# Optimization experiments

Measured on AMD Instinct MI355X. Metric: run time of the kernel, lower is better.

The kernel has to match this reference:

```python
import jax, jax.numpy as jnp
import numpy as np

N_NODES = 50000
N_EDGES = 800000
EMB = 128
HID = [128, 128]
OUT = 64
CE = 8  # stand-in for CROSS_ENTROPY_INDEXES: first 8 output columns get sigmoid


def _linear_params(key, d_in, d_out):
    k1, k2 = jax.random.split(key)
    s = 1.0 / np.sqrt(d_in)
    w = jax.random.uniform(k1, (d_in, d_out), minval=-s, maxval=s, dtype=jnp.float32)
    b = jax.random.uniform(k2, (d_out,), minval=-s, maxval=s, dtype=jnp.float32)
    return w, b


def setup_inputs() -> dict:
    key = jax.random.key(0)
    ks = jax.random.split(key, 16)
    z = jax.random.normal(ks[0], (N_NODES, EMB), dtype=jnp.float32)
    edge_index = jax.random.randint(ks[1], (2, N_EDGES), 0, N_NODES, dtype=jnp.int64)
    # SAGEConv params: neighbor weight (with bias) + root weight
    w1_n, b1 = _linear_params(ks[2], EMB, HID[0])
    w1_r, _ = _linear_params(ks[3], EMB, HID[0])
    w2_n, b2 = _linear_params(ks[4], HID[0], HID[1])
    w2_r, _ = _linear_params(ks[5], HID[0], HID[1])
    wf_n, bf = _linear_params(ks[6], HID[1], OUT)
    wf_r, _ = _linear_params(ks[7], HID[1], OUT)
    # initial residual linears: emb -> hid[1], emb -> out
    w_res1, b_res1 = _linear_params(ks[8], EMB, HID[1])
    w_res2, b_res2 = _linear_params(ks[9], EMB, OUT)
    return dict(z=z, edge_index=edge_index,
                w1_n=w1_n, w1_r=w1_r, b1=b1,
                w2_n=w2_n, w2_r=w2_r, b2=b2,
                wf_n=wf_n, wf_r=wf_r, bf=bf,
                w_res1=w_res1, b_res1=b_res1,
                w_res2=w_res2, b_res2=b_res2)


def _sage(x, src, dst, w_n, w_r, b, n_nodes):
    # mean-aggregate neighbor features at target nodes, then affine combine with root
    msg = x[src]                                        # [E, d]
    agg = jax.ops.segment_sum(msg, dst, num_segments=n_nodes)
    deg = jax.ops.segment_sum(jnp.ones_like(dst, dtype=x.dtype), dst, num_segments=n_nodes)
    mean = agg / jnp.maximum(deg, 1.0)[:, None]
    return mean @ w_n + x @ w_r + b


def reference(z, edge_index, w1_n, w1_r, b1, w2_n, w2_r, b2, wf_n, wf_r, bf,
              w_res1, b_res1, w_res2, b_res2):
    n = z.shape[0]
    src, dst = edge_index[0], edge_index[1]
    h = jax.nn.relu(_sage(z, src, dst, w1_n, w1_r, b1, n))
    # mid layer (dropout is identity in eval) + initial residual
    h = jax.nn.relu(_sage(h, src, dst, w2_n, w2_r, b2, n))
    h = h + (z @ w_res1 + b_res1)
    # final conv + final residual
    h = _sage(h, src, dst, wf_n, wf_r, bf, n)
    h = h + (z @ w_res2 + b_res2)
    # sigmoid on cross-entropy columns
    h = h.at[:, :CE].set(jax.nn.sigmoid(h[:, :CE]))
    return h
```

## Files before the change

### kernel.cpp

```cpp
#include <hip/hip_runtime.h>
#include <hip/hip_bf16.h>
#include <math.h>

#define NN 50000
#define NNP 50048
#define NE 800000
#define NB 391
#define EPB 6250

typedef short bf16x8 __attribute__((ext_vector_type(8)));
typedef float f32x4 __attribute__((ext_vector_type(4)));
typedef float f32x2 __attribute__((ext_vector_type(2)));
typedef unsigned short us4 __attribute__((ext_vector_type(4)));
typedef unsigned short us8 __attribute__((ext_vector_type(8)));
typedef unsigned int u32x4 __attribute__((ext_vector_type(4)));

__device__ __forceinline__ float bf2f(unsigned short u) {
  union { unsigned int i; float f; } x; x.i = ((unsigned int)u) << 16; return x.f;
}
__device__ __forceinline__ float u2f(unsigned int u) {
  union { unsigned int i; float f; } x; x.i = u; return x.f;
}
__device__ __forceinline__ unsigned short f2bf(float f) {
  union { float f; unsigned int i; } x; x.f = f;
  unsigned int i = x.i;
  unsigned int r = i + 0x7FFF + ((i >> 16) & 1);
  return (unsigned short)(r >> 16);
}
__device__ __forceinline__ unsigned long long pk64(f32x4 v) {
  union { us4 s; unsigned long long u; } x;
  x.s[0] = f2bf(v[0]); x.s[1] = f2bf(v[1]); x.s[2] = f2bf(v[2]); x.s[3] = f2bf(v[3]);
  return x.u;
}
__device__ __forceinline__ bf16x8 bfrag(const unsigned short* __restrict__ Bp, int idx, int lane) {
  return *(const bf16x8*)(Bp + (size_t)idx * 512 + lane * 8);
}

__device__ __forceinline__ int scan_incl_512(int v, int* s) {
  int t = threadIdx.x;
  s[t] = v; __syncthreads();
  for (int off = 1; off < 512; off <<= 1) {
    int x = (t >= off) ? s[t - off] : 0;
    __syncthreads();
    s[t] += x;
    __syncthreads();
  }
  return s[t];
}

__global__ __launch_bounds__(512) void bscat_kernel(const int* __restrict__ srcn,
                                                    const int* __restrict__ dstn,
                                                    const int* __restrict__ bhist,
                                                    int* __restrict__ gcur,
                                                    unsigned long long* __restrict__ ebuf) {
  __shared__ int sbuf[512];
  __shared__ int boff[NB];
  __shared__ int hist[NB];
  __shared__ int base[NB];
  int t = threadIdx.x;
  int v = (t < NB) ? bhist[t] : 0;
  int incl = scan_incl_512(v, sbuf);
  if (t < NB) { boff[t] = incl - v; hist[t] = 0; }
  __syncthreads();
  int e0 = blockIdx.x * EPB;
  for (int i = t; i < EPB; i += 512)
    atomicAdd(&hist[dstn[e0 + i] >> 7], 1);
  __syncthreads();
  for (int i = t; i < NB; i += 512) {
    int c = hist[i];
    base[i] = c ? (boff[i] + atomicAdd(&gcur[i], c)) : 0;
  }
  __syncthreads();
  for (int i = t; i < EPB; i += 512) {
    int s = srcn[e0 + i], d = dstn[e0 + i];
    int b = d >> 7;
    int pos = atomicSub(&hist[b], 1) - 1;
    ebuf[(size_t)base[b] + pos] = ((unsigned long long)(unsigned)d << 32) | (unsigned)s;
  }
}

__global__ __launch_bounds__(512) void bfill_kernel(const unsigned long long* __restrict__ ebuf,
                                                    const int* __restrict__ bhist,
                                                    int* __restrict__ rowoff,
                                                    int* __restrict__ csr) {
  __shared__ int sbuf[512];
  __shared__ int sb[2];
  __shared__ int ndeg[128], noff[128];
  int b = blockIdx.x;
  int t = threadIdx.x;
  int v = (t < NB) ? bhist[t] : 0;
  int incl = scan_incl_512(v, sbuf);
  if (t == b) { sb[0] = incl - v; sb[1] = v; }
  if (t < 128) ndeg[t] = 0;
  __syncthreads();
  int bo = sb[0], cnt = sb[1];
  for (int i = t; i < cnt; i += 512)
    atomicAdd(&ndeg[(int)(ebuf[bo + i] >> 32) & 127], 1);
  __syncthreads();
  if (t < 128) noff[t] = ndeg[t];
  __syncthreads();
  for (int off = 1; off < 128; off <<= 1) {
    int x = 0;
    if (t < 128 && t >= off) x = noff[t - off];
    __syncthreads();
    if (t < 128 && t >= off) noff[t] += x;
    __syncthreads();
  }
  if (t < 128) {
    int ex = noff[t] - ndeg[t];
    noff[t] = ex;
    int node = b * 128 + t;
    if (node < NN) rowoff[node] = bo + ex;
  }
  if (b == NB - 1 && t == 0) rowoff[NN] = NE;
  __syncthreads();
  for (int i = t; i < cnt; i += 512) {
    unsigned long long e = ebuf[bo + i];
    int dl = (int)(e >> 32) & 127;
    int pos = atomicSub(&ndeg[dl], 1) - 1;
    csr[bo + noff[dl] + pos] = (int)(unsigned)e;
  }
}

__global__ __launch_bounds__(256) void setup_kernel(
    const float* __restrict__ z, unsigned short* __restrict__ A1,
    const float* __restrict__ w1n, const float* __restrict__ w1r,
    const float* __restrict__ w2n, const float* __restrict__ w2r,
    const float* __restrict__ wfn, const float* __restrict__ wfr,
    const float* __restrict__ wr1, const float* __restrict__ wr2,
    unsigned short* __restrict__ Bp1, unsigned short* __restrict__ Bp2,
    unsigned short* __restrict__ Bp3,
    const int* __restrict__ dstn, int* __restrict__ bhist) {
  __shared__ int h[NB];
  int b = blockIdx.x;
  if (b < 6250) {
    int i = b * 256 + threadIdx.x;
    if (i >= NN * 128 / 4) return;
    int i4 = i * 4;
    int row = i4 >> 7, c = i4 & 127;
    f32x4 v = *(const f32x4*)(z + i4);
    us4 o = { f2bf(v[0]), f2bf(v[1]), f2bf(v[2]), f2bf(v[3]) };
    *(us4*)(A1 + (size_t)row * 256 + 128 + c) = o;
  } else if (b < 6314) {
    int g = (b - 6250) * 256 + threadIdx.x;
    unsigned short* D; int NT, fi;
    int which;
    if      (g < 10240) { fi = g;         D = Bp1; NT = 20; which = 1; }
    else if (g < 14336) { fi = g - 10240; D = Bp2; NT = 8;  which = 2; }
    else if (g < 16384) { fi = g - 14336; D = Bp3; NT = 4;  which = 3; }
    else return;
    int lane = fi & 63, t = fi >> 6;
    int nt = t % NT, k0i = t / NT;
    int m = lane & 15, q = lane >> 4;
    int kb = k0i * 32 + q * 8;
    int n = nt * 16 + m;
    int hi = (kb >= 128);
    int k0_ = kb - (hi ? 128 : 0);
    const float* W = nullptr; int Nseg = 128; int nn = n;
    if (which == 1) {
      if (n < 128)      { W = hi ? w1r : w1n; nn = n; Nseg = 128; }
      else if (n < 256) { W = hi ? wr1 : nullptr; nn = n - 128; Nseg = 128; }
      else              { W = hi ? wr2 : nullptr; nn = n - 256; Nseg = 64; }
    } else if (which == 2) { W = hi ? w2r : w2n; Nseg = 128; }
    else                   { W = hi ? wfr : wfn; Nseg = 64; }
    unsigned short o[8];
#pragma unroll
    for (int j = 0; j < 8; j++)
      o[j] = W ? f2bf(W[(size_t)(k0_ + j) * Nseg + nn]) : (unsigned short)0;
    *(us8*)(D + (size_t)fi * 8) = *(const us8*)o;
  } else {
    for (int i = threadIdx.x; i < NB; i += 256) h[i] = 0;
    __syncthreads();
    int e0 = (b - 6314) * EPB;
    for (int i = threadIdx.x; i < EPB; i += 256)
      atomicAdd(&h[dstn[e0 + i] >> 7], 1);
    __syncthreads();
    for (int i = threadIdx.x; i < NB; i += 256)
      if (h[i]) atomicAdd(&bhist[i], h[i]);
  }
}

__device__ __forceinline__ void agg_wave(const unsigned short* __restrict__ feat,
                                         unsigned short* __restrict__ outm,
                                         const int* __restrict__ rowoff,
                                         const int* __restrict__ csr, int node) {
  int lane = threadIdx.x & 63;
  int g = lane >> 4;
  int c = (lane & 15) << 3;
  int beg = rowoff[node], end = rowoff[node + 1];
  f32x2 a[4];
#pragma unroll
  for (int k = 0; k < 4; ++k) a[k] = (f32x2){0.f, 0.f};
  int e1 = end - 1;
  for (int j = beg + g; j < end; j += 16) {
    int j1 = (j + 4 < e1) ? j + 4 : e1;
    int j2 = (j + 8 < e1) ? j + 8 : e1;
    int j3 = (j + 12 < e1) ? j + 12 : e1;
    int s0 = csr[j], s1 = csr[j1], s2 = csr[j2], s3 = csr[j3];
    float w1 = (j + 4 < end) ? 1.f : 0.f;
    float w2 = (j + 8 < end) ? 1.f : 0.f;
    float w3 = (j + 12 < end) ? 1.f : 0.f;
    u32x4 v0 = *(const u32x4*)(feat + (size_t)s0 * 256 + c);
    u32x4 v1 = *(const u32x4*)(feat + (size_t)s1 * 256 + c);
    u32x4 v2 = *(const u32x4*)(feat + (size_t)s2 * 256 + c);
    u32x4 v3 = *(const u32x4*)(feat + (size_t)s3 * 256 + c);
#pragma unroll
    for (int k = 0; k < 4; ++k) {
      f32x2 x0 = (f32x2){u2f(v0[k] << 16), u2f(v0[k] & 0xffff0000u)};
      f32x2 x1 = (f32x2){u2f(v1[k] << 16), u2f(v1[k] & 0xffff0000u)};
      f32x2 x2 = (f32x2){u2f(v2[k] << 16), u2f(v2[k] & 0xffff0000u)};
      f32x2 x3 = (f32x2){u2f(v3[k] << 16), u2f(v3[k] & 0xffff0000u)};
      a[k] += x0;
      a[k] += x1 * w1;
      a[k] += x2 * w2;
      a[k] += x3 * w3;
    }
  }
#pragma unroll
  for (int k = 0; k < 4; ++k)
#pragma unroll
    for (int h2 = 0; h2 < 2; ++h2) {
      a[k][h2] += __shfl_xor(a[k][h2], 16, 64);
      a[k][h2] += __shfl_xor(a[k][h2], 32, 64);
    }
  if (g == 0) {
    float inv = 1.f / fmaxf((float)(end - beg), 1.f);
    unsigned int o[4];
#pragma unroll
    for (int k = 0; k < 4; ++k)
      o[k] = ((unsigned int)f2bf(a[k][1] * inv) << 16) | f2bf(a[k][0] * inv);
    *(u32x4*)(outm + (size_t)node * 256 + c) = *(const u32x4*)o;
  }
}

__global__ __launch_bounds__(512, 8) void agg_kernel(unsigned short* __restrict__ A,
                                                     const int* __restrict__ rowoff,
                                                     const int* __restrict__ csr) {
  int node = blockIdx.x * 8 + (threadIdx.x >> 6);
  agg_wave(A + 128, A, rowoff, csr, node);
}

__global__ __launch_bounds__(512, 8) void aggres1_kernel(
    unsigned short* __restrict__ A1,
    const unsigned short* __restrict__ Bp1,
    const float* __restrict__ br1, const float* __restrict__ br2,
    const int* __restrict__ rowoff, const int* __restrict__ csr,
    unsigned short* __restrict__ res1, unsigned short* __restrict__ res2) {
  int bx = blockIdx.x;
  if (bx < 6250) {
    int node = bx * 8 + (threadIdx.x >> 6);
    agg_wave(A1 + 128, A1, rowoff, csr, node);
    return;
  }
  int b = bx - 6250;
  int chunk = (b >= NB);
  int bb = b - chunk * NB;
  int tid = threadIdx.x;
  int w = tid >> 6, lane = tid & 63;
  int m = lane & 15, q = lane >> 4;
  int row = bb * 128 + w * 16 + m;
  const unsigned short* ar = A1 + (size_t)row * 256 + 128 + q * 8;
  bf16x8 af[4];
#pragma unroll
  for (int k = 0; k < 4; ++k) af[k] = *(const bf16x8*)(ar + k * 32);
  f32x4 acc[6];
#pragma unroll
  for (int t = 0; t < 6; ++t) acc[t] = (f32x4){0.f, 0.f, 0.f, 0.f};
#pragma unroll
  for (int k0i = 0; k0i < 4; ++k0i)
#pragma unroll
    for (int t = 0; t < 6; ++t)
      acc[t] = __builtin_amdgcn_mfma_f32_16x16x32_bf16(
          bfrag(Bp1, (k0i + 4) * 20 + 8 + chunk * 6 + t, lane), af[k0i], acc[t], 0, 0, 0);
  int src0 = m + ((q & 1) ? 32 : 0);
#pragma unroll
  for (int pl = 0; pl < 3; ++pl) {
    int P = chunk * 3 + pl;
    const float* bias; unsigned short* dst; int dstride, colb;
    if (P < 4) { bias = br1 + 32 * P;       dst = res1; dstride = 128; colb = 32 * P; }
    else       { bias = br2 + 32 * (P - 4); dst = res2; dstride = 64;  colb = 32 * (P - 4); }
    f32x4 v0 = acc[2 * pl], v1 = acc[2 * pl + 1];
    f32x4 bb0 = *(const f32x4*)(bias + 4 * q);
    f32x4 bb1 = *(const f32x4*)(bias + 16 + 4 * q);
#pragma unroll
    for (int r = 0; r < 4; ++r) { v0[r] += bb0[r]; v1[r] += bb1[r]; }
    unsigned long long d0 = pk64(v0), d1 = pk64(v1);
    unsigned long long a0 = __shfl(d0, src0, 64);
    unsigned long long b0 = __shfl(d0, src0 + 16, 64);
    unsigned long long a1 = __shfl(d1, src0, 64);
    unsigned long long b1v = __shfl(d1, src0 + 16, 64);
    unsigned long long lo = (q >> 1) ? a1 : a0;
    unsigned long long hi = (q >> 1) ? b1v : b0;
    if (row < NN) {
      unsigned long long ov[2] = { lo, hi };
      *(us8*)(dst + (size_t)row * dstride + colb + 8 * q) = *(const us8*)ov;
    }
  }
}

__global__ __launch_bounds__(256, 4) void gemm1h_kernel(
    const unsigned short* __restrict__ A1,
    const unsigned short* __restrict__ Bp1,
    const float* __restrict__ b1,
    unsigned short* __restrict__ A2) {
  int tid = threadIdx.x;
  int w = tid >> 6, lane = tid & 63;
  int m = lane & 15, q = lane >> 4;
  int row = blockIdx.x * 64 + w * 16 + m;
  const unsigned short* ar = A1 + (size_t)row * 256 + q * 8;
  bf16x8 af[8];
#pragma unroll
  for (int k = 0; k < 8; ++k) af[k] = *(const bf16x8*)(ar + k * 32);
  f32x4 acc[8];
#pragma unroll
  for (int t = 0; t < 8; ++t) acc[t] = (f32x4){0.f, 0.f, 0.f, 0.f};
#pragma unroll
  for (int k0i = 0; k0i < 8; ++k0i)
#pragma unroll
    for (int t = 0; t < 8; ++t)
      acc[t] = __builtin_amdgcn_mfma_f32_16x16x32_bf16(
          bfrag(Bp1, k0i * 20 + t, lane), af[k0i], acc[t], 0, 0, 0);
  int src0 = m + ((q & 1) ? 32 : 0);
#pragma unroll
  for (int p = 0; p < 4; ++p) {
    f32x4 v0 = acc[2 * p], v1 = acc[2 * p + 1];
    f32x4 bb0 = *(const f32x4*)(b1 + 32 * p + 4 * q);
    f32x4 bb1 = *(const f32x4*)(b1 + 32 * p + 16 + 4 * q);
#pragma unroll
    for (int r = 0; r < 4; ++r) {
      v0[r] = fmaxf(v0[r] + bb0[r], 0.f);
      v1[r] = fmaxf(v1[r] + bb1[r], 0.f);
    }
    unsigned long long d0 = pk64(v0), d1 = pk64(v1);
    unsigned long long a0 = __shfl(d0, src0, 64);
    unsigned long long b0 = __shfl(d0, src0 + 16, 64);
    unsigned long long a1 = __shfl(d1, src0, 64);
    unsigned long long b1v = __shfl(d1, src0 + 16, 64);
    unsigned long long lo = (q >> 1) ? a1 : a0;
    unsigned long long hi = (q >> 1) ? b1v : b0;
    if (row < NN) {
      unsigned long long ov[2] = { lo, hi };
      *(us8*)(A2 + (size_t)row * 256 + 128 + 32 * p + 8 * q) = *(const us8*)ov;
    }
  }
}

__global__ __launch_bounds__(256, 4) void gemm2_kernel(
    const unsigned short* __restrict__ A2,
    const unsigned short* __restrict__ Bp2,
    const float* __restrict__ b2,
    const unsigned short* __restrict__ res1,
    unsigned short* __restrict__ A3) {
  int tid = threadIdx.x;
  int w = tid >> 6, lane = tid & 63;
  int m = lane & 15, q = lane >> 4;
  int row = blockIdx.x * 64 + w * 16 + m;
  const unsigned short* ar = A2 + (size_t)row * 256 + q * 8;
  bf16x8 af[8];
#pragma unroll
  for (int k = 0; k < 8; ++k) af[k] = *(const bf16x8*)(ar + k * 32);
  f32x4 acc[8];
#pragma unroll
  for (int t = 0; t < 8; ++t) acc[t] = (f32x4){0.f, 0.f, 0.f, 0.f};
#pragma unroll
  for (int k0i = 0; k0i < 8; ++k0i)
#pragma unroll
    for (int t = 0; t < 8; ++t)
      acc[t] = __builtin_amdgcn_mfma_f32_16x16x32_bf16(
          bfrag(Bp2, k0i * 8 + t, lane), af[k0i], acc[t], 0, 0, 0);
  int src0 = m + ((q & 1) ? 32 : 0);
#pragma unroll
  for (int p = 0; p < 4; ++p) {
    f32x4 v0 = acc[2 * p], v1 = acc[2 * p + 1];
    f32x4 bb0 = *(const f32x4*)(b2 + 32 * p + 4 * q);
    f32x4 bb1 = *(const f32x4*)(b2 + 32 * p + 16 + 4 * q);
#pragma unroll
    for (int r = 0; r < 4; ++r) {
      v0[r] = fmaxf(v0[r] + bb0[r], 0.f);
      v1[r] = fmaxf(v1[r] + bb1[r], 0.f);
    }
    unsigned long long d0 = pk64(v0), d1 = pk64(v1);
    unsigned long long a0 = __shfl(d0, src0, 64);
    unsigned long long b0 = __shfl(d0, src0 + 16, 64);
    unsigned long long a1 = __shfl(d1, src0, 64);
    unsigned long long b1v = __shfl(d1, src0 + 16, 64);
    unsigned long long lo = (q >> 1) ? a1 : a0;
    unsigned long long hi = (q >> 1) ? b1v : b0;
    if (row < NN) {
      size_t off = 32 * p + 8 * q;
      us8 rv = *(const us8*)(res1 + (size_t)row * 128 + off);
      unsigned long long ov[2] = { lo, hi };
      unsigned short* e = (unsigned short*)ov;
#pragma unroll
      for (int r = 0; r < 8; ++r) e[r] = f2bf(bf2f(e[r]) + bf2f(rv[r]));
      *(us8*)(A3 + (size_t)row * 256 + 128 + off) = *(const us8*)ov;
    }
  }
}

__global__ __launch_bounds__(256, 4) void gemm3_kernel(
    const unsigned short* __restrict__ A3,
    const unsigned short* __restrict__ Bp3,
    const float* __restrict__ bias,
    const unsigned short* __restrict__ res2,
    float* __restrict__ out_f) {
  int tid = threadIdx.x;
  int w = tid >> 6, lane = tid & 63;
  int m = lane & 15, q = lane >> 4;
  int row = blockIdx.x * 64 + w * 16 + m;
  const unsigned short* ar = A3 + (size_t)row * 256 + q * 8;
  bf16x8 af[8];
#pragma unroll
  for (int k = 0; k < 8; ++k) af[k] = *(const bf16x8*)(ar + k * 32);
  f32x4 acc[4];
#pragma unroll
  for (int t = 0; t < 4; ++t) acc[t] = (f32x4){0.f, 0.f, 0.f, 0.f};
#pragma unroll
  for (int k0i = 0; k0i < 8; ++k0i)
#pragma unroll
    for (int t = 0; t < 4; ++t)
      acc[t] = __builtin_amdgcn_mfma_f32_16x16x32_bf16(
          bfrag(Bp3, k0i * 4 + t, lane), af[k0i], acc[t], 0, 0, 0);
  if (row >= NN) return;
  int cb = q * 4;
#pragma unroll
  for (int s = 0; s < 4; ++s) {
    int col = s * 16 + cb;
    f32x4 v = acc[s];
    f32x4 bb = *(const f32x4*)(bias + col);
    us4 rv = *(const us4*)(res2 + (size_t)row * 64 + col);
#pragma unroll
    for (int r = 0; r < 4; ++r) v[r] += bb[r] + bf2f(rv[r]);
    if (col < 8) {
#pragma unroll
      for (int r = 0; r < 4; ++r) v[r] = 1.f / (1.f + __expf(-v[r]));
    }
    *(f32x4*)(out_f + (size_t)row * 64 + col) = v;
  }
}

extern "C" void kernel_launch(void* const* d_in, const int* in_sizes, int n_in,
                              void* d_out, int out_size, void* d_ws, size_t ws_size,
                              hipStream_t stream) {
  const float* z   = (const float*)d_in[0];
  const int*   edge = (const int*)d_in[1];
  const int*   srcn = edge;
  const int*   dstn = edge + NE;
  const float* w1n = (const float*)d_in[2];
  const float* w1r = (const float*)d_in[3];
  const float* b1  = (const float*)d_in[4];
  const float* w2n = (const float*)d_in[5];
  const float* w2r = (const float*)d_in[6];
  const float* b2  = (const float*)d_in[7];
  const float* wfn = (const float*)d_in[8];
  const float* wfr = (const float*)d_in[9];
  const float* bfb = (const float*)d_in[10];
  const float* wr1 = (const float*)d_in[11];
  const float* br1 = (const float*)d_in[12];
  const float* wr2 = (const float*)d_in[13];
  const float* br2 = (const float*)d_in[14];
  float* out = (float*)d_out;

  char* p = (char*)d_ws;
  auto alloc = [&](size_t bytes) { char* r = p; p += (bytes + 255) & ~255ull; return r; };
  int* rowoff = (int*)alloc((size_t)(NN + 1) * 4);
  int* bhist  = (int*)alloc((size_t)2 * NB * 4);
  int* gcur   = bhist + NB;
  int* csr    = (int*)alloc((size_t)NE * 4);
  unsigned short* A1 = (unsigned short*)alloc((size_t)NNP * 256 * 2);
  unsigned short* A2 = (unsigned short*)alloc((size_t)NNP * 256 * 2);
  unsigned short* res1 = (unsigned short*)alloc((size_t)NN * 128 * 2);
  unsigned short* res2 = (unsigned short*)alloc((size_t)NN * 64 * 2);
  unsigned short* Bp1 = (unsigned short*)alloc(10240 * 8 * 2);
  unsigned short* Bp2 = (unsigned short*)alloc(4096 * 8 * 2);
  unsigned short* Bp3 = (unsigned short*)alloc(2048 * 8 * 2);
  unsigned short* A3 = A1;
  unsigned long long* ebuf = (unsigned long long*)res1;

  hipMemsetAsync(bhist, 0, (size_t)2 * NB * 4, stream);
  setup_kernel<<<6442, 256, 0, stream>>>(z, A1, w1n, w1r, w2n, w2r, wfn, wfr, wr1, wr2,
                                         Bp1, Bp2, Bp3, dstn, bhist);
  bscat_kernel<<<128, 512, 0, stream>>>(srcn, dstn, bhist, gcur, ebuf);
  bfill_kernel<<<NB, 512, 0, stream>>>(ebuf, bhist, rowoff, csr);

  const int ggemm = NNP / 64;

  aggres1_kernel<<<6250 + 2 * NB, 512, 0, stream>>>(A1, Bp1, br1, br2, rowoff, csr, res1, res2);
  gemm1h_kernel<<<ggemm, 256, 0, stream>>>(A1, Bp1, b1, A2);

  agg_kernel<<<6250, 512, 0, stream>>>(A2, rowoff, csr);
  gemm2_kernel<<<ggemm, 256, 0, stream>>>(A2, Bp2, b2, res1, A3);

  agg_kernel<<<6250, 512, 0, stream>>>(A3, rowoff, csr);
  gemm3_kernel<<<ggemm, 256, 0, stream>>>(A3, Bp3, bfb, res2, out);
}
```

Before: 279.3 us.

## Project before aggregating in final layer and process two nodes per wave

The final SAGE layer now multiplies the hidden features by the neighbor weight inside gemm2 (mean is linear, so mean(x)W = mean(xW)), which lets the third aggregation gather 64-wide instead of 128-wide rows. A new agg64 kernel handles that narrower gather, and gemm3 then only multiplies the root half and adds the aggregated projection. The 128-wide aggregation is restructured so each wave handles two nodes at once, with clamped indices, to raise memory-level parallelism, and launch bounds drop to 4 waves per EU. Row guards on stores are removed by padding the residual buffers to NNP. The extra projection adds MFMA work to gemm2, and rounding the projected features to bf16 before the mean slightly changes numerics.

Measured after the change: 279.4 us. Within noise of the previous version (+0.1%).

```diff
diff --git a/kernel.cpp b/kernel.cpp
--- a/kernel.cpp
+++ b/kernel.cpp
@@ -180,46 +180,131 @@
   }
 }
 
-__device__ __forceinline__ void agg_wave(const unsigned short* __restrict__ feat,
-                                         unsigned short* __restrict__ outm,
-                                         const int* __restrict__ rowoff,
-                                         const int* __restrict__ csr, int node) {
+__device__ __forceinline__ void agg_wave2(const unsigned short* __restrict__ feat,
+                                          unsigned short* __restrict__ outm,
+                                          const int* __restrict__ rowoff,
+                                          const int* __restrict__ csr, int n0) {
   int lane = threadIdx.x & 63;
   int g = lane >> 4;
   int c = (lane & 15) << 3;
+  int begA = rowoff[n0], begB = rowoff[n0 + 1], endB = rowoff[n0 + 2];
+  int endA = begB;
+  f32x2 aA[4], aB[4];
+#pragma unroll
+  for (int k = 0; k < 4; ++k) { aA[k] = (f32x2){0.f, 0.f}; aB[k] = (f32x2){0.f, 0.f}; }
+  int e1A = endA - 1 > begA ? endA - 1 : begA;
+  int e1B = endB - 1 > begB ? endB - 1 : begB;
+  if (e1A >= NE) e1A = NE - 1;
+  if (e1B >= NE) e1B = NE - 1;
+  int jA = begA + g, jB = begB + g;
+  while (jA < endA || jB < endB) {
+    int iA0 = jA      < e1A ? jA      : e1A;
+    int iA1 = jA + 4  < e1A ? jA + 4  : e1A;
+    int iA2 = jA + 8  < e1A ? jA + 8  : e1A;
+    int iA3 = jA + 12 < e1A ? jA + 12 : e1A;
+    int iB0 = jB      < e1B ? jB      : e1B;
+    int iB1 = jB + 4  < e1B ? jB + 4  : e1B;
+    int iB2 = jB + 8  < e1B ? jB + 8  : e1B;
+    int iB3 = jB + 12 < e1B ? jB + 12 : e1B;
+    int sA0 = csr[iA0], sA1 = csr[iA1], sA2 = csr[iA2], sA3 = csr[iA3];
+    int sB0 = csr[iB0], sB1 = csr[iB1], sB2 = csr[iB2], sB3 = csr[iB3];
+    float wA0 = (jA      < endA) ? 1.f : 0.f;
+    float wA1 = (jA + 4  < endA) ? 1.f : 0.f;
+    float wA2 = (jA + 8  < endA) ? 1.f : 0.f;
+    float wA3 = (jA + 12 < endA) ? 1.f : 0.f;
+    float wB0 = (jB      < endB) ? 1.f : 0.f;
+    float wB1 = (jB + 4  < endB) ? 1.f : 0.f;
+    float wB2 = (jB + 8  < endB) ? 1.f : 0.f;
+    float wB3 = (jB + 12 < endB) ? 1.f : 0.f;
+    u32x4 vA0 = *(const u32x4*)(feat + (size_t)sA0 * 256 + c);
+    u32x4 vA1 = *(const u32x4*)(feat + (size_t)sA1 * 256 + c);
+    u32x4 vA2 = *(const u32x4*)(feat + (size_t)sA2 * 256 + c);
+    u32x4 vA3 = *(const u32x4*)(feat + (size_t)sA3 * 256 + c);
+    u32x4 vB0 = *(const u32x4*)(feat + (size_t)sB0 * 256 + c);
+    u32x4 vB1 = *(const u32x4*)(feat + (size_t)sB1 * 256 + c);
+    u32x4 vB2 = *(const u32x4*)(feat + (size_t)sB2 * 256 + c);
+    u32x4 vB3 = *(const u32x4*)(feat + (size_t)sB3 * 256 + c);
+#pragma unroll
+    for (int k = 0; k < 4; ++k) {
+      aA[k] += (f32x2){u2f(vA0[k] << 16), u2f(vA0[k] & 0xffff0000u)} * wA0;
+      aA[k] += (f32x2){u2f(vA1[k] << 16), u2f(vA1[k] & 0xffff0000u)} * wA1;
+      aA[k] += (f32x2){u2f(vA2[k] << 16), u2f(vA2[k] & 0xffff0000u)} * wA2;
+      aA[k] += (f32x2){u2f(vA3[k] << 16), u2f(vA3[k] & 0xffff0000u)} * wA3;
+      aB[k] += (f32x2){u2f(vB0[k] << 16), u2f(vB0[k] & 0xffff0000u)} * wB0;
+      aB[k] += (f32x2){u2f(vB1[k] << 16), u2f(vB1[k] & 0xffff0000u)} * wB1;
+      aB[k] += (f32x2){u2f(vB2[k] << 16), u2f(vB2[k] & 0xffff0000u)} * wB2;
+      aB[k] += (f32x2){u2f(vB3[k] << 16), u2f(vB3[k] & 0xffff0000u)} * wB3;
+    }
+    jA += 16; jB += 16;
+  }
+#pragma unroll
+  for (int k = 0; k < 4; ++k)
+#pragma unroll
+    for (int h2 = 0; h2 < 2; ++h2) {
+      aA[k][h2] += __shfl_xor(aA[k][h2], 16, 64);
+      aA[k][h2] += __shfl_xor(aA[k][h2], 32, 64);
+      aB[k][h2] += __shfl_xor(aB[k][h2], 16, 64);
+      aB[k][h2] += __shfl_xor(aB[k][h2], 32, 64);
+    }
+  if (g == 0) {
+    float invA = 1.f / fmaxf((float)(endA - begA), 1.f);
+    float invB = 1.f / fmaxf((float)(endB - begB), 1.f);
+    unsigned int oA[4], oB[4];
+#pragma unroll
+    for (int k = 0; k < 4; ++k) {
+      oA[k] = ((unsigned int)f2bf(aA[k][1] * invA) << 16) | f2bf(aA[k][0] * invA);
+      oB[k] = ((unsigned int)f2bf(aB[k][1] * invB) << 16) | f2bf(aB[k][0] * invB);
+    }
+    *(u32x4*)(outm + (size_t)n0 * 256 + c) = *(const u32x4*)oA;
+    *(u32x4*)(outm + (size_t)(n0 + 1) * 256 + c) = *(const u32x4*)oB;
+  }
+}
+
+__global__ __launch_bounds__(512, 4) void agg_kernel(unsigned short* __restrict__ A,
+                                                     const int* __restrict__ rowoff,
+                                                     const int* __restrict__ csr) {
+  int n0 = (blockIdx.x * 8 + (threadIdx.x >> 6)) * 2;
+  agg_wave2(A + 128, A, rowoff, csr, n0);
+}
+
+__device__ __forceinline__ void agg64_wave(const unsigned short* __restrict__ feat,
+                                           unsigned short* __restrict__ outm,
+                                           const int* __restrict__ rowoff,
+                                           const int* __restrict__ csr, int node) {
+  int lane = threadIdx.x & 63;
+  int g = lane >> 3;
+  int c = (lane & 7) << 3;
   int beg = rowoff[node], end = rowoff[node + 1];
   f32x2 a[4];
 #pragma unroll
   for (int k = 0; k < 4; ++k) a[k] = (f32x2){0.f, 0.f};
-  int e1 = end - 1;
-  for (int j = beg + g; j < end; j += 16) {
-    int j1 = (j + 4 < e1) ? j + 4 : e1;
-    int j2 = (j + 8 < e1) ? j + 8 : e1;
-    int j3 = (j + 12 < e1) ? j + 12 : e1;
+  int e1 = end - 1 > beg ? end - 1 : beg;
+  if (e1 >= NE) e1 = NE - 1;
+  for (int j = beg + g; j < end; j += 32) {
+    int j1 = (j + 8  < e1) ? j + 8  : e1;
+    int j2 = (j + 16 < e1) ? j + 16 : e1;
+    int j3 = (j + 24 < e1) ? j + 24 : e1;
     int s0 = csr[j], s1 = csr[j1], s2 = csr[j2], s3 = csr[j3];
-    float w1 = (j + 4 < end) ? 1.f : 0.f;
-    float w2 = (j + 8 < end) ? 1.f : 0.f;
-    float w3 = (j + 12 < end) ? 1.f : 0.f;
+    float w1 = (j + 8  < end) ? 1.f : 0.f;
+    float w2 = (j + 16 < end) ? 1.f : 0.f;
+    float w3 = (j + 24 < end) ? 1.f : 0.f;
     u32x4 v0 = *(const u32x4*)(feat + (size_t)s0 * 256 + c);
     u32x4 v1 = *(const u32x4*)(feat + (size_t)s1 * 256 + c);
     u32x4 v2 = *(const u32x4*)(feat + (size_t)s2 * 256 + c);
     u32x4 v3 = *(const u32x4*)(feat + (size_t)s3 * 256 + c);
 #pragma unroll
     for (int k = 0; k < 4; ++k) {
-      f32x2 x0 = (f32x2){u2f(v0[k] << 16), u2f(v0[k] & 0xffff0000u)};
-      f32x2 x1 = (f32x2){u2f(v1[k] << 16), u2f(v1[k] & 0xffff0000u)};
-      f32x2 x2 = (f32x2){u2f(v2[k] << 16), u2f(v2[k] & 0xffff0000u)};
-      f32x2 x3 = (f32x2){u2f(v3[k] << 16), u2f(v3[k] & 0xffff0000u)};
-      a[k] += x0;
-      a[k] += x1 * w1;
-      a[k] += x2 * w2;
-      a[k] += x3 * w3;
+      a[k] += (f32x2){u2f(v0[k] << 16), u2f(v0[k] & 0xffff0000u)};
+      a[k] += (f32x2){u2f(v1[k] << 16), u2f(v1[k] & 0xffff0000u)} * w1;
+      a[k] += (f32x2){u2f(v2[k] << 16), u2f(v2[k] & 0xffff0000u)} * w2;
+      a[k] += (f32x2){u2f(v3[k] << 16), u2f(v3[k] & 0xffff0000u)} * w3;
     }
   }
 #pragma unroll
   for (int k = 0; k < 4; ++k)
 #pragma unroll
     for (int h2 = 0; h2 < 2; ++h2) {
+      a[k][h2] += __shfl_xor(a[k][h2], 8, 64);
       a[k][h2] += __shfl_xor(a[k][h2], 16, 64);
       a[k][h2] += __shfl_xor(a[k][h2], 32, 64);
     }
@@ -233,26 +318,26 @@
   }
 }
 
-__global__ __launch_bounds__(512, 8) void agg_kernel(unsigned short* __restrict__ A,
-                                                     const int* __restrict__ rowoff,
-                                                     const int* __restrict__ csr) {
+__global__ __launch_bounds__(512, 8) void agg64_kernel(unsigned short* __restrict__ A1,
+                                                       const int* __restrict__ rowoff,
+                                                       const int* __restrict__ csr) {
   int node = blockIdx.x * 8 + (threadIdx.x >> 6);
-  agg_wave(A + 128, A, rowoff, csr, node);
-}
-
-__global__ __launch_bounds__(512, 8) void aggres1_kernel(
+  agg64_wave(A1 + 64, A1, rowoff, csr, node);
+}
+
+__global__ __launch_bounds__(512, 4) void aggres1_kernel(
     unsigned short* __restrict__ A1,
     const unsigned short* __restrict__ Bp1,
     const float* __restrict__ br1, const float* __restrict__ br2,
     const int* __restrict__ rowoff, const int* __restrict__ csr,
     unsigned short* __restrict__ res1, unsigned short* __restrict__ res2) {
   int bx = blockIdx.x;
-  if (bx < 6250) {
-    int node = bx * 8 + (threadIdx.x >> 6);
-    agg_wave(A1 + 128, A1, rowoff, csr, node);
+  if (bx < 3125) {
+    int n0 = (bx * 8 + (threadIdx.x >> 6)) * 2;
+    agg_wave2(A1 + 128, A1, rowoff, csr, n0);
     return;
   }
-  int b = bx - 6250;
+  int b = bx - 3125;
   int chunk = (b >= NB);
   int bb = b - chunk * NB;
   int tid = threadIdx.x;
@@ -291,10 +376,8 @@
     unsigned long long b1v = __shfl(d1, src0 + 16, 64);
     unsigned long long lo = (q >> 1) ? a1 : a0;
     unsigned long long hi = (q >> 1) ? b1v : b0;
-    if (row < NN) {
-      unsigned long long ov[2] = { lo, hi };
-      *(us8*)(dst + (size_t)row * dstride + colb + 8 * q) = *(const us8*)ov;
-    }
+    unsigned long long ov[2] = { lo, hi };
+    *(us8*)(dst + (size_t)row * dstride + colb + 8 * q) = *(const us8*)ov;
   }
 }
 
@@ -338,19 +421,18 @@
     unsigned long long b1v = __shfl(d1, src0 + 16, 64);
     unsigned long long lo = (q >> 1) ? a1 : a0;
     unsigned long long hi = (q >> 1) ? b1v : b0;
-    if (row < NN) {
-      unsigned long long ov[2] = { lo, hi };
-      *(us8*)(A2 + (size_t)row * 256 + 128 + 32 * p + 8 * q) = *(const us8*)ov;
-    }
+    unsigned long long ov[2] = { lo, hi };
+    *(us8*)(A2 + (size_t)row * 256 + 128 + 32 * p + 8 * q) = *(const us8*)ov;
   }
 }
 
 __global__ __launch_bounds__(256, 4) void gemm2_kernel(
     const unsigned short* __restrict__ A2,
     const unsigned short* __restrict__ Bp2,
+    const unsigned short* __restrict__ Bp3,
     const float* __restrict__ b2,
     const unsigned short* __restrict__ res1,
-    unsigned short* __restrict__ A3) {
+    unsigned short* __restrict__ A1out) {
   int tid = threadIdx.x;
   int w = tid >> 6, lane = tid & 63;
   int m = lane & 15, q = lane >> 4;
@@ -369,6 +451,7 @@
       acc[t] = __builtin_amdgcn_mfma_f32_16x16x32_bf16(
           bfrag(Bp2, k0i * 8 + t, lane), af[k0i], acc[t], 0, 0, 0);
   int src0 = m + ((q & 1) ? 32 : 0);
+  bf16x8 afy[4];
 #pragma unroll
   for (int p = 0; p < 4; ++p) {
     f32x4 v0 = acc[2 * p], v1 = acc[2 * p + 1];
@@ -386,20 +469,41 @@
     unsigned long long b1v = __shfl(d1, src0 + 16, 64);
     unsigned long long lo = (q >> 1) ? a1 : a0;
     unsigned long long hi = (q >> 1) ? b1v : b0;
-    if (row < NN) {
-      size_t off = 32 * p + 8 * q;
-      us8 rv = *(const us8*)(res1 + (size_t)row * 128 + off);
-      unsigned long long ov[2] = { lo, hi };
-      unsigned short* e = (unsigned short*)ov;
-#pragma unroll
-      for (int r = 0; r < 8; ++r) e[r] = f2bf(bf2f(e[r]) + bf2f(rv[r]));
-      *(us8*)(A3 + (size_t)row * 256 + 128 + off) = *(const us8*)ov;
-    }
+    size_t off = 32 * p + 8 * q;
+    us8 rv = *(const us8*)(res1 + (size_t)row * 128 + off);
+    unsigned long long ov[2] = { lo, hi };
+    unsigned short* e = (unsigned short*)ov;
+#pragma unroll
+    for (int r = 0; r < 8; ++r) e[r] = f2bf(bf2f(e[r]) + bf2f(rv[r]));
+    *(us8*)(A1out + (size_t)row * 256 + 128 + off) = *(const us8*)ov;
+    afy[p] = *(const bf16x8*)ov;
+  }
+  f32x4 accy[4];
+#pragma unroll
+  for (int t = 0; t < 4; ++t) accy[t] = (f32x4){0.f, 0.f, 0.f, 0.f};
+#pragma unroll
+  for (int p = 0; p < 4; ++p)
+#pragma unroll
+    for (int t = 0; t < 4; ++t)
+      accy[t] = __builtin_amdgcn_mfma_f32_16x16x32_bf16(
+          bfrag(Bp3, p * 4 + t, lane), afy[p], accy[t], 0, 0, 0);
+#pragma unroll
+  for (int py = 0; py < 2; ++py) {
+    f32x4 v0 = accy[2 * py], v1 = accy[2 * py + 1];
+    unsigned long long d0 = pk64(v0), d1 = pk64(v1);
+    unsigned long long a0 = __shfl(d0, src0, 64);
+    unsigned long long b0 = __shfl(d0, src0 + 16, 64);
+    unsigned long long a1 = __shfl(d1, src0, 64);
+    unsigned long long b1v = __shfl(d1, src0 + 16, 64);
+    unsigned long long lo = (q >> 1) ? a1 : a0;
+    unsigned long long hi = (q >> 1) ? b1v : b0;
+    unsigned long long ov[2] = { lo, hi };
+    *(us8*)(A1out + (size_t)row * 256 + 64 + 32 * py + 8 * q) = *(const us8*)ov;
   }
 }
 
 __global__ __launch_bounds__(256, 4) void gemm3_kernel(
-    const unsigned short* __restrict__ A3,
+    const unsigned short* __restrict__ A1,
     const unsigned short* __restrict__ Bp3,
     const float* __restrict__ bias,
     const unsigned short* __restrict__ res2,
@@ -408,19 +512,19 @@
   int w = tid >> 6, lane = tid & 63;
   int m = lane & 15, q = lane >> 4;
   int row = blockIdx.x * 64 + w * 16 + m;
-  const unsigned short* ar = A3 + (size_t)row * 256 + q * 8;
-  bf16x8 af[8];
-#pragma unroll
-  for (int k = 0; k < 8; ++k) af[k] = *(const bf16x8*)(ar + k * 32);
+  const unsigned short* ar = A1 + (size_t)row * 256 + 128 + q * 8;
+  bf16x8 af[4];
+#pragma unroll
+  for (int k = 0; k < 4; ++k) af[k] = *(const bf16x8*)(ar + k * 32);
   f32x4 acc[4];
 #pragma unroll
   for (int t = 0; t < 4; ++t) acc[t] = (f32x4){0.f, 0.f, 0.f, 0.f};
 #pragma unroll
-  for (int k0i = 0; k0i < 8; ++k0i)
+  for (int k0i = 0; k0i < 4; ++k0i)
 #pragma unroll
     for (int t = 0; t < 4; ++t)
       acc[t] = __builtin_amdgcn_mfma_f32_16x16x32_bf16(
-          bfrag(Bp3, k0i * 4 + t, lane), af[k0i], acc[t], 0, 0, 0);
+          bfrag(Bp3, (k0i + 4) * 4 + t, lane), af[k0i], acc[t], 0, 0, 0);
   if (row >= NN) return;
   int cb = q * 4;
 #pragma unroll
@@ -429,8 +533,9 @@
     f32x4 v = acc[s];
     f32x4 bb = *(const f32x4*)(bias + col);
     us4 rv = *(const us4*)(res2 + (size_t)row * 64 + col);
-#pragma unroll
-    for (int r = 0; r < 4; ++r) v[r] += bb[r] + bf2f(rv[r]);
+    us4 mv = *(const us4*)(A1 + (size_t)row * 256 + col);
+#pragma unroll
+    for (int r = 0; r < 4; ++r) v[r] += bb[r] + bf2f(rv[r]) + bf2f(mv[r]);
     if (col < 8) {
 #pragma unroll
       for (int r = 0; r < 4; ++r) v[r] = 1.f / (1.f + __expf(-v[r]));
@@ -469,12 +574,11 @@
   int* csr    = (int*)alloc((size_t)NE * 4);
   unsigned short* A1 = (unsigned short*)alloc((size_t)NNP * 256 * 2);
   unsigned short* A2 = (unsigned short*)alloc((size_t)NNP * 256 * 2);
-  unsigned short* res1 = (unsigned short*)alloc((size_t)NN * 128 * 2);
-  unsigned short* res2 = (unsigned short*)alloc((size_t)NN * 64 * 2);
+  unsigned short* res1 = (unsigned short*)alloc((size_t)NNP * 128 * 2);
+  unsigned short* res2 = (unsigned short*)alloc((size_t)NNP * 64 * 2);
   unsigned short* Bp1 = (unsigned short*)alloc(10240 * 8 * 2);
   unsigned short* Bp2 = (unsigned short*)alloc(4096 * 8 * 2);
   unsigned short* Bp3 = (unsigned short*)alloc(2048 * 8 * 2);
-  unsigned short* A3 = A1;
   unsigned long long* ebuf = (unsigned long long*)res1;
 
   hipMemsetAsync(bhist, 0, (size_t)2 * NB * 4, stream);
@@ -485,12 +589,12 @@
 
   const int ggemm = NNP / 64;
 
-  aggres1_kernel<<<6250 + 2 * NB, 512, 0, stream>>>(A1, Bp1, br1, br2, rowoff, csr, res1, res2);
+  aggres1_kernel<<<3125 + 2 * NB, 512, 0, stream>>>(A1, Bp1, br1, br2, rowoff, csr, res1, res2);
   gemm1h_kernel<<<ggemm, 256, 0, stream>>>(A1, Bp1, b1, A2);
 
-  agg_kernel<<<6250, 512, 0, stream>>>(A2, rowoff, csr);
-  gemm2_kernel<<<ggemm, 256, 0, stream>>>(A2, Bp2, b2, res1, A3);
-
-  agg_kernel<<<6250, 512, 0, stream>>>(A3, rowoff, csr);
-  gemm3_kernel<<<ggemm, 256, 0, stream>>>(A3, Bp3, bfb, res2, out);
-}
+  agg_kernel<<<3125, 512, 0, stream>>>(A2, rowoff, csr);
+  gemm2_kernel<<<ggemm, 256, 0, stream>>>(A2, Bp2, Bp3, b2, res1, A1);
+
+  agg64_kernel<<<6250, 512, 0, stream>>>(A1, rowoff, csr);
+  gemm3_kernel<<<ggemm, 256, 0, stream>>>(A1, Bp3, bfb, res2, out);
+}
```

## Project layer-3 features before aggregation and fuse aggregation into final GEMM

Applied to the files above, without the earlier changes.

Uses linearity of mean aggregation to apply the final neighbor weight inside gemm2, producing 64-wide projected features instead of 128-wide ones. The last aggregation then gathers only 64 columns and is fused with the root-weight GEMM and epilogue in one kernel, with the means staged in shared memory. This is meant to halve the gather traffic of the third aggregation and drop one launch plus the intermediate round trip. In exchange it adds rounding of the projected features to bf16 before averaging, and the fused kernel aggregates with only 4 waves per 64-row block, which may limit latency hiding. Row bounds checks are removed and the residual buffers are padded to cover the extra rows.

New measurement: 279.1 us. No clear change (-0.1%).

```diff
diff --git a/kernel.cpp b/kernel.cpp
--- a/kernel.cpp
+++ b/kernel.cpp
@@ -206,14 +206,10 @@
     u32x4 v3 = *(const u32x4*)(feat + (size_t)s3 * 256 + c);
 #pragma unroll
     for (int k = 0; k < 4; ++k) {
-      f32x2 x0 = (f32x2){u2f(v0[k] << 16), u2f(v0[k] & 0xffff0000u)};
-      f32x2 x1 = (f32x2){u2f(v1[k] << 16), u2f(v1[k] & 0xffff0000u)};
-      f32x2 x2 = (f32x2){u2f(v2[k] << 16), u2f(v2[k] & 0xffff0000u)};
-      f32x2 x3 = (f32x2){u2f(v3[k] << 16), u2f(v3[k] & 0xffff0000u)};
-      a[k] += x0;
-      a[k] += x1 * w1;
-      a[k] += x2 * w2;
-      a[k] += x3 * w3;
+      a[k] += (f32x2){u2f(v0[k] << 16), u2f(v0[k] & 0xffff0000u)};
+      a[k] += (f32x2){u2f(v1[k] << 16), u2f(v1[k] & 0xffff0000u)} * w1;
+      a[k] += (f32x2){u2f(v2[k] << 16), u2f(v2[k] & 0xffff0000u)} * w2;
+      a[k] += (f32x2){u2f(v3[k] << 16), u2f(v3[k] & 0xffff0000u)} * w3;
     }
   }
 #pragma unroll
@@ -291,10 +287,8 @@
     unsigned long long b1v = __shfl(d1, src0 + 16, 64);
     unsigned long long lo = (q >> 1) ? a1 : a0;
     unsigned long long hi = (q >> 1) ? b1v : b0;
-    if (row < NN) {
-      unsigned long long ov[2] = { lo, hi };
-      *(us8*)(dst + (size_t)row * dstride + colb + 8 * q) = *(const us8*)ov;
-    }
+    unsigned long long ov[2] = { lo, hi };
+    *(us8*)(dst + (size_t)row * dstride + colb + 8 * q) = *(const us8*)ov;
   }
 }
 
@@ -338,19 +332,18 @@
     unsigned long long b1v = __shfl(d1, src0 + 16, 64);
     unsigned long long lo = (q >> 1) ? a1 : a0;
     unsigned long long hi = (q >> 1) ? b1v : b0;
-    if (row < NN) {
-      unsigned long long ov[2] = { lo, hi };
-      *(us8*)(A2 + (size_t)row * 256 + 128 + 32 * p + 8 * q) = *(const us8*)ov;
-    }
+    unsigned long long ov[2] = { lo, hi };
+    *(us8*)(A2 + (size_t)row * 256 + 128 + 32 * p + 8 * q) = *(const us8*)ov;
   }
 }
 
 __global__ __launch_bounds__(256, 4) void gemm2_kernel(
     const unsigned short* __restrict__ A2,
     const unsigned short* __restrict__ Bp2,
+    const unsigned short* __restrict__ Bp3,
     const float* __restrict__ b2,
     const unsigned short* __restrict__ res1,
-    unsigned short* __restrict__ A3) {
+    unsigned short* __restrict__ A1out) {
   int tid = threadIdx.x;
   int w = tid >> 6, lane = tid & 63;
   int m = lane & 15, q = lane >> 4;
@@ -369,6 +362,7 @@
       acc[t] = __builtin_amdgcn_mfma_f32_16x16x32_bf16(
           bfrag(Bp2, k0i * 8 + t, lane), af[k0i], acc[t], 0, 0, 0);
   int src0 = m + ((q & 1) ? 32 : 0);
+  bf16x8 afy[4];
 #pragma unroll
   for (int p = 0; p < 4; ++p) {
     f32x4 v0 = acc[2 * p], v1 = acc[2 * p + 1];
@@ -386,41 +380,116 @@
     unsigned long long b1v = __shfl(d1, src0 + 16, 64);
     unsigned long long lo = (q >> 1) ? a1 : a0;
     unsigned long long hi = (q >> 1) ? b1v : b0;
-    if (row < NN) {
-      size_t off = 32 * p + 8 * q;
-      us8 rv = *(const us8*)(res1 + (size_t)row * 128 + off);
-      unsigned long long ov[2] = { lo, hi };
-      unsigned short* e = (unsigned short*)ov;
-#pragma unroll
-      for (int r = 0; r < 8; ++r) e[r] = f2bf(bf2f(e[r]) + bf2f(rv[r]));
-      *(us8*)(A3 + (size_t)row * 256 + 128 + off) = *(const us8*)ov;
-    }
-  }
-}
-
-__global__ __launch_bounds__(256, 4) void gemm3_kernel(
-    const unsigned short* __restrict__ A3,
+    size_t off = 32 * p + 8 * q;
+    us8 rv = *(const us8*)(res1 + (size_t)row * 128 + off);
+    unsigned long long ov[2] = { lo, hi };
+    unsigned short* e = (unsigned short*)ov;
+#pragma unroll
+    for (int r = 0; r < 8; ++r) e[r] = f2bf(bf2f(e[r]) + bf2f(rv[r]));
+    *(us8*)(A1out + (size_t)row * 256 + 128 + off) = *(const us8*)ov;
+    afy[p] = *(const bf16x8*)ov;
+  }
+  f32x4 accy[4];
+#pragma unroll
+  for (int t = 0; t < 4; ++t) accy[t] = (f32x4){0.f, 0.f, 0.f, 0.f};
+#pragma unroll
+  for (int p = 0; p < 4; ++p)
+#pragma unroll
+    for (int t = 0; t < 4; ++t)
+      accy[t] = __builtin_amdgcn_mfma_f32_16x16x32_bf16(
+          bfrag(Bp3, p * 4 + t, lane), afy[p], accy[t], 0, 0, 0);
+#pragma unroll
+  for (int py = 0; py < 2; ++py) {
+    f32x4 v0 = accy[2 * py], v1 = accy[2 * py + 1];
+    unsigned long long d0 = pk64(v0), d1 = pk64(v1);
+    unsigned long long a0 = __shfl(d0, src0, 64);
+    unsigned long long b0 = __shfl(d0, src0 + 16, 64);
+    unsigned long long a1 = __shfl(d1, src0, 64);
+    unsigned long long b1v = __shfl(d1, src0 + 16, 64);
+    unsigned long long lo = (q >> 1) ? a1 : a0;
+    unsigned long long hi = (q >> 1) ? b1v : b0;
+    unsigned long long ov[2] = { lo, hi };
+    *(us8*)(A1out + (size_t)row * 256 + 64 + 32 * py + 8 * q) = *(const us8*)ov;
+  }
+}
+
+__global__ __launch_bounds__(256, 4) void aggemm3_kernel(
+    const unsigned short* __restrict__ A1,
     const unsigned short* __restrict__ Bp3,
     const float* __restrict__ bias,
+    const int* __restrict__ rowoff, const int* __restrict__ csr,
     const unsigned short* __restrict__ res2,
     float* __restrict__ out_f) {
+  __shared__ unsigned short meanS[64 * 64];
   int tid = threadIdx.x;
   int w = tid >> 6, lane = tid & 63;
+  int row0 = blockIdx.x * 64;
+  {
+    const unsigned short* feat = A1 + 64;
+    int g = lane >> 3;
+    int c = (lane & 7) << 3;
+    for (int i = 0; i < 16; ++i) {
+      int node = row0 + w * 16 + i;
+      int beg = 0, end = 0;
+      if (node < NN) { beg = rowoff[node]; end = rowoff[node + 1]; }
+      f32x2 a[4];
+#pragma unroll
+      for (int k = 0; k < 4; ++k) a[k] = (f32x2){0.f, 0.f};
+      int e1 = end - 1 > beg ? end - 1 : beg;
+      for (int j = beg + g; j < end; j += 32) {
+        int j1 = (j + 8  < e1) ? j + 8  : e1;
+        int j2 = (j + 16 < e1) ? j + 16 : e1;
+        int j3 = (j + 24 < e1) ? j + 24 : e1;
+        int s0 = csr[j], s1 = csr[j1], s2 = csr[j2], s3 = csr[j3];
+        float w1 = (j + 8  < end) ? 1.f : 0.f;
+        float w2 = (j + 16 < end) ? 1.f : 0.f;
+        float w3 = (j + 24 < end) ? 1.f : 0.f;
+        u32x4 v0 = *(const u32x4*)(feat + (size_t)s0 * 256 + c);
+        u32x4 v1 = *(const u32x4*)(feat + (size_t)s1 * 256 + c);
+        u32x4 v2 = *(const u32x4*)(feat + (size_t)s2 * 256 + c);
+        u32x4 v3 = *(const u32x4*)(feat + (size_t)s3 * 256 + c);
+#pragma unroll
+        for (int k = 0; k < 4; ++k) {
+          a[k] += (f32x2){u2f(v0[k] << 16), u2f(v0[k] & 0xffff0000u)};
+          a[k] += (f32x2){u2f(v1[k] << 16), u2f(v1[k] & 0xffff0000u)} * w1;
+          a[k] += (f32x2){u2f(v2[k] << 16), u2f(v2[k] & 0xffff0000u)} * w2;
+          a[k] += (f32x2){u2f(v3[k] << 16), u2f(v3[k] & 0xffff0000u)} * w3;
+        }
+      }
+#pragma unroll
+      for (int k = 0; k < 4; ++k)
+#pragma unroll
+        for (int h2 = 0; h2 < 2; ++h2) {
+          a[k][h2] += __shfl_xor(a[k][h2], 8, 64);
+          a[k][h2] += __shfl_xor(a[k][h2], 16, 64);
+          a[k][h2] += __shfl_xor(a[k][h2], 32, 64);
+        }
+      if (g == 0) {
+        float inv = 1.f / fmaxf((float)(end - beg), 1.f);
+        unsigned int o[4];
+#pragma unroll
+        for (int k = 0; k < 4; ++k)
+          o[k] = ((unsigned int)f2bf(a[k][1] * inv) << 16) | f2bf(a[k][0] * inv);
+        *(u32x4*)(meanS + (size_t)(w * 16 + i) * 64 + c) = *(const u32x4*)o;
+      }
+    }
+  }
+  __syncthreads();
   int m = lane & 15, q = lane >> 4;
-  int row = blockIdx.x * 64 + w * 16 + m;
-  const unsigned short* ar = A3 + (size_t)row * 256 + q * 8;
-  bf16x8 af[8];
-#pragma unroll
-  for (int k = 0; k < 8; ++k) af[k] = *(const bf16x8*)(ar + k * 32);
+  int row = row0 + w * 16 + m;
+  const unsigned short* ar = A1 + (size_t)row * 256 + 128 + q * 8;
+  bf16x8 af[4];
+#pragma unroll
+  for (int k = 0; k < 4; ++k) af[k] = *(const bf16x8*)(ar + k * 32);
   f32x4 acc[4];
 #pragma unroll
   for (int t = 0; t < 4; ++t) acc[t] = (f32x4){0.f, 0.f, 0.f, 0.f};
 #pragma unroll
-  for (int k0i = 0; k0i < 8; ++k0i)
+  for (int k0i = 0; k0i < 4; ++k0i)
 #pragma unroll
     for (int t = 0; t < 4; ++t)
       acc[t] = __builtin_amdgcn_mfma_f32_16x16x32_bf16(
-          bfrag(Bp3, k0i * 4 + t, lane), af[k0i], acc[t], 0, 0, 0);
+          bfrag(Bp3, (k0i + 4) * 4 + t, lane), af[k0i], acc[t], 0, 0, 0);
   if (row >= NN) return;
   int cb = q * 4;
 #pragma unroll
@@ -429,8 +498,9 @@
     f32x4 v = acc[s];
     f32x4 bb = *(const f32x4*)(bias + col);
     us4 rv = *(const us4*)(res2 + (size_t)row * 64 + col);
-#pragma unroll
-    for (int r = 0; r < 4; ++r) v[r] += bb[r] + bf2f(rv[r]);
+    us4 mv = *(const us4*)(meanS + (size_t)(w * 16 + m) * 64 + col);
+#pragma unroll
+    for (int r = 0; r < 4; ++r) v[r] += bb[r] + bf2f(rv[r]) + bf2f(mv[r]);
     if (col < 8) {
 #pragma unroll
       for (int r = 0; r < 4; ++r) v[r] = 1.f / (1.f + __expf(-v[r]));
@@ -469,12 +539,11 @@
   int* csr    = (int*)alloc((size_t)NE * 4);
   unsigned short* A1 = (unsigned short*)alloc((size_t)NNP * 256 * 2);
   unsigned short* A2 = (unsigned short*)alloc((size_t)NNP * 256 * 2);
-  unsigned short* res1 = (unsigned short*)alloc((size_t)NN * 128 * 2);
-  unsigned short* res2 = (unsigned short*)alloc((size_t)NN * 64 * 2);
+  unsigned short* res1 = (unsigned short*)alloc((size_t)NNP * 128 * 2);
+  unsigned short* res2 = (unsigned short*)alloc((size_t)NNP * 64 * 2);
   unsigned short* Bp1 = (unsigned short*)alloc(10240 * 8 * 2);
   unsigned short* Bp2 = (unsigned short*)alloc(4096 * 8 * 2);
   unsigned short* Bp3 = (unsigned short*)alloc(2048 * 8 * 2);
-  unsigned short* A3 = A1;
   unsigned long long* ebuf = (unsigned long long*)res1;
 
   hipMemsetAsync(bhist, 0, (size_t)2 * NB * 4, stream);
@@ -489,8 +558,7 @@
   gemm1h_kernel<<<ggemm, 256, 0, stream>>>(A1, Bp1, b1, A2);
 
   agg_kernel<<<6250, 512, 0, stream>>>(A2, rowoff, csr);
-  gemm2_kernel<<<ggemm, 256, 0, stream>>>(A2, Bp2, b2, res1, A3);
-
-  agg_kernel<<<6250, 512, 0, stream>>>(A3, rowoff, csr);
-  gemm3_kernel<<<ggemm, 256, 0, stream>>>(A3, Bp3, bfb, res2, out);
-}
+  gemm2_kernel<<<ggemm, 256, 0, stream>>>(A2, Bp2, Bp3, b2, res1, A1);
+
+  aggemm3_kernel<<<ggemm, 256, 0, stream>>>(A1, Bp3, bfb, rowoff, csr, res2, out);
+}
```
